# Performance work log

Hardware: AMD Instinct MI355X
Metric: run time of the kernel (lower is better)

## Reference

```python
import jax, jax.numpy as jnp
import numpy as np

TOKENS = 1024
HIDDEN = 1024
INTER = 4096
N_EXPERTS = 8


def setup_inputs() -> dict:
    key = jax.random.key(0)
    k1, k2, k3, k4 = jax.random.split(key, 4)
    hidden_states = jax.random.normal(k1, (TOKENS, HIDDEN), dtype=jnp.float32)
    # multi-hot expert assignment mask [tokens, num_experts] with values in {0,1}
    expert_indices = jax.random.randint(k2, (TOKENS, N_EXPERTS), 0, 2, dtype=jnp.int32)
    # Phi3MLP weights per expert (Linear layers have bias=False in Phi3)
    scale_gu = 1.0 / np.sqrt(HIDDEN)
    scale_d = 1.0 / np.sqrt(INTER)
    w_gate_up = jax.random.normal(k3, (N_EXPERTS, HIDDEN, 2 * INTER), dtype=jnp.float32) * scale_gu
    w_down = jax.random.normal(k4, (N_EXPERTS, INTER, HIDDEN), dtype=jnp.float32) * scale_d
    return {
        "hidden_states": hidden_states,
        "expert_indices": expert_indices,
        "w_gate_up": w_gate_up,
        "w_down": w_down,
    }


def reference(hidden_states, expert_indices, w_gate_up, w_down):
    # Original loops per expert: gather masked tokens, run Phi3MLP, scatter-add back.
    # Mathematically equivalent dense form (jit-friendly, static shapes):
    #   out = sum_e mask[:, e] * Phi3MLP_e(x)
    # gate_up: [E, T, 2*I]
    gu = jnp.einsum('th,ehi->eti', hidden_states, w_gate_up)
    gate, up = jnp.split(gu, 2, axis=-1)  # each [E, T, I]
    act = up * jax.nn.silu(gate)          # Phi3MLP: up * silu(gate)
    y = jnp.einsum('eti,eih->eth', act, w_down)  # [E, T, H]
    mask = expert_indices.astype(hidden_states.dtype)  # [T, E]
    out = jnp.einsum('eth,te->th', y, mask)
    return out
```

## Files before the change

kernel.cpp:

```cpp
#include <hip/hip_runtime.h>
#include <hip/hip_bf16.h>
#include <stdint.h>

#define T_TOK 1024
#define HID   1024
#define INT_  4096
#define NE    8

typedef __attribute__((ext_vector_type(4))) float f32x4;
typedef __attribute__((ext_vector_type(8))) short short8;

__device__ int g_tok[NE][T_TOK];
__device__ int g_cnt[NE];

__device__ __forceinline__ uint32_t pack2bf(float a, float b) {
  unsigned short ua = __builtin_bit_cast(unsigned short, (__bf16)a);
  unsigned short ub = __builtin_bit_cast(unsigned short, (__bf16)b);
  return (uint32_t)ua | ((uint32_t)ub << 16);
}

#define GL16(gsrc, ldst)                                                       \
  __builtin_amdgcn_global_load_lds(                                            \
      (const __attribute__((address_space(1))) void*)(gsrc),                   \
      (__attribute__((address_space(3))) void*)(ldst), 16, 0, 0)

__global__ void k0_compact(const int* __restrict__ mask)
{
  const int w    = threadIdx.x >> 6;
  const int lane = threadIdx.x & 63;
  if (w >= NE) return;
  const unsigned long long ltmask = (1ull << lane) - 1ull;
  int base = 0;
  #pragma unroll
  for (int c = 0; c < T_TOK / 64; ++c) {
    const int t = c * 64 + lane;
    const bool pred = mask[t * NE + w] != 0;
    const unsigned long long bal = __ballot(pred);
    if (pred) g_tok[w][base + __popcll(bal & ltmask)] = t;
    base += __popcll(bal);
  }
  if (lane == 0) g_cnt[w] = base;
}

__global__ void cvt_x(const float* __restrict__ xin, unsigned short* __restrict__ xout)
{
  const int i = (blockIdx.x * 256 + threadIdx.x) * 8;
  f32x4 a = *(const f32x4*)(xin + i);
  f32x4 b = *(const f32x4*)(xin + i + 4);
  uint4 u;
  u.x = pack2bf(a[0], a[1]); u.y = pack2bf(a[2], a[3]);
  u.z = pack2bf(b[0], b[1]); u.w = pack2bf(b[2], b[3]);
  *(uint4*)(xout + i) = u;
}

__global__ void cvt_T(const float* __restrict__ in, unsigned short* __restrict__ out,
                      int R, int C)
{
  __shared__ float tile[64][65];
  const int e  = blockIdx.z;
  const int c0 = blockIdx.x * 64;
  const int r0 = blockIdx.y * 64;
  const float*    ip = in  + (size_t)e * R * C;
  unsigned short* op = out + (size_t)e * R * C;
  const int t  = threadIdx.x;
  const int rr = t >> 4, c4 = (t & 15) * 4;
  #pragma unroll
  for (int s = 0; s < 4; ++s) {
    f32x4 v = *(const f32x4*)(ip + (size_t)(r0 + s * 16 + rr) * C + c0 + c4);
    tile[s * 16 + rr][c4 + 0] = v[0];
    tile[s * 16 + rr][c4 + 1] = v[1];
    tile[s * 16 + rr][c4 + 2] = v[2];
    tile[s * 16 + rr][c4 + 3] = v[3];
  }
  __syncthreads();
  const int c = t >> 2, rs = (t & 3) * 16;
  uint4 u0, u1;
  u0.x = pack2bf(tile[rs + 0][c],  tile[rs + 1][c]);
  u0.y = pack2bf(tile[rs + 2][c],  tile[rs + 3][c]);
  u0.z = pack2bf(tile[rs + 4][c],  tile[rs + 5][c]);
  u0.w = pack2bf(tile[rs + 6][c],  tile[rs + 7][c]);
  u1.x = pack2bf(tile[rs + 8][c],  tile[rs + 9][c]);
  u1.y = pack2bf(tile[rs + 10][c], tile[rs + 11][c]);
  u1.z = pack2bf(tile[rs + 12][c], tile[rs + 13][c]);
  u1.w = pack2bf(tile[rs + 14][c], tile[rs + 15][c]);
  unsigned short* orow = op + (size_t)(c0 + c) * R + r0 + rs;
  *(uint4*)(orow)     = u0;
  *(uint4*)(orow + 8) = u1;
}

__global__ __launch_bounds__(512, 1)
void k1_gateup(const unsigned short* __restrict__ xb,
               const unsigned short* __restrict__ wguT,
               unsigned short* __restrict__ act)
{
  const int e   = blockIdx.z;
  const int cnt = g_cnt[e];
  const int mt  = blockIdx.y;
  const int t0  = mt * 256;
  if (t0 >= cnt) return;

  __shared__ char sA [256 * 128];
  __shared__ char sBg[128 * 128];
  __shared__ char sBu[128 * 128];

  const int nt   = blockIdx.x;
  const int tid  = threadIdx.x;
  const int lane = tid & 63;
  const int wv   = tid >> 6;
  const int wm   = (wv >> 2) * 128;
  const int wn   = (wv & 3) * 32;
  const int n0   = nt * 128;

  const unsigned short* wg = wguT + (size_t)e * 8192 * HID + (size_t)n0 * HID;
  const unsigned short* wu = wg + (size_t)4096 * HID;

  f32x4 accg[8][2], accu[8][2];
  #pragma unroll
  for (int i = 0; i < 8; ++i)
    #pragma unroll
    for (int j = 0; j < 2; ++j) {
      accg[i][j] = (f32x4){0.f, 0.f, 0.f, 0.f};
      accu[i][j] = (f32x4){0.f, 0.f, 0.f, 0.f};
    }

  const int drow  = lane >> 3;
  const int dchk8 = (((lane & 7) ^ drow) << 3);

  int tokA[4];
  #pragma unroll
  for (int s = 0; s < 4; ++s)
    tokA[s] = g_tok[e][t0 + (s * 8 + wv) * 8 + drow];

  for (int kt = 0; kt < HID; kt += 64) {
    #pragma unroll
    for (int s = 0; s < 4; ++s) {
      const int rb = (s * 8 + wv) * 8;
      GL16(xb + (size_t)tokA[s] * HID + kt + dchk8, sA + rb * 128);
    }
    #pragma unroll
    for (int s = 0; s < 2; ++s) {
      const int rb = (s * 8 + wv) * 8;
      GL16(wg + (size_t)(rb + drow) * HID + kt + dchk8, sBg + rb * 128);
      GL16(wu + (size_t)(rb + drow) * HID + kt + dchk8, sBu + rb * 128);
    }
    __syncthreads();
    #pragma unroll
    for (int ks = 0; ks < 2; ++ks) {
      const int kfb = ks * 64 + ((lane >> 4) << 4);
      short8 af[8], bg[2], bu[2];
      #pragma unroll
      for (int i = 0; i < 8; ++i) {
        const int r = wm + i * 16 + (lane & 15);
        af[i] = *(const short8*)(sA + r * 128 + (kfb ^ ((r & 7) << 4)));
      }
      #pragma unroll
      for (int j = 0; j < 2; ++j) {
        const int r = wn + j * 16 + (lane & 15);
        const int off = r * 128 + (kfb ^ ((r & 7) << 4));
        bg[j] = *(const short8*)(sBg + off);
        bu[j] = *(const short8*)(sBu + off);
      }
      #pragma unroll
      for (int i = 0; i < 8; ++i)
        #pragma unroll
        for (int j = 0; j < 2; ++j) {
          accg[i][j] = __builtin_amdgcn_mfma_f32_16x16x32_bf16(af[i], bg[j], accg[i][j], 0, 0, 0);
          accu[i][j] = __builtin_amdgcn_mfma_f32_16x16x32_bf16(af[i], bu[j], accu[i][j], 0, 0, 0);
        }
    }
    __syncthreads();
  }

  unsigned short* ab = act + (size_t)e * T_TOK * INT_;
  #pragma unroll
  for (int i = 0; i < 8; ++i) {
    #pragma unroll
    for (int r = 0; r < 4; ++r) {
      const int slot = t0 + wm + i * 16 + ((lane >> 4) << 2) + r;
      if (slot < cnt) {
        #pragma unroll
        for (int j = 0; j < 2; ++j) {
          const int col = n0 + wn + j * 16 + (lane & 15);
          const float g = accg[i][j][r];
          const float u = accu[i][j][r];
          const float s = u * g / (1.f + __expf(-g));
          ab[(size_t)slot * INT_ + col] = __builtin_bit_cast(unsigned short, (__bf16)s);
        }
      }
    }
  }
}

__global__ __launch_bounds__(256, 2)
void k2_down(const unsigned short* __restrict__ act,
             const unsigned short* __restrict__ wdT,
             float* __restrict__ out)
{
  const int e   = blockIdx.z;
  const int cnt = g_cnt[e];
  const int mt  = blockIdx.y >> 2;
  const int ks4 = blockIdx.y & 3;
  const int t0  = mt * 128;
  if (t0 >= cnt) return;

  __shared__ char sA[128 * 128];
  __shared__ char sB[128 * 128];

  const int nt   = blockIdx.x;
  const int tid  = threadIdx.x;
  const int lane = tid & 63;
  const int wv   = tid >> 6;
  const int wm   = (wv >> 1) * 64;
  const int wn   = (wv & 1) * 64;
  const int n0   = nt * 128;

  const unsigned short* ab = act + (size_t)e * T_TOK * INT_;
  const unsigned short* wb = wdT + (size_t)e * HID * INT_ + (size_t)n0 * INT_;

  f32x4 acc[4][4];
  #pragma unroll
  for (int i = 0; i < 4; ++i)
    #pragma unroll
    for (int j = 0; j < 4; ++j) acc[i][j] = (f32x4){0.f, 0.f, 0.f, 0.f};

  const int drow  = lane >> 3;
  const int dchk8 = (((lane & 7) ^ drow) << 3);

  const int kbeg = ks4 * (INT_ / 4);

  for (int kt = kbeg; kt < kbeg + INT_ / 4; kt += 64) {
    #pragma unroll
    for (int s = 0; s < 4; ++s) {
      const int rb = (s * 4 + wv) * 8;
      GL16(ab + (size_t)(t0 + rb + drow) * INT_ + kt + dchk8, sA + rb * 128);
      GL16(wb + (size_t)(rb + drow) * INT_ + kt + dchk8, sB + rb * 128);
    }
    __syncthreads();
    #pragma unroll
    for (int ks = 0; ks < 2; ++ks) {
      const int kfb = ks * 64 + ((lane >> 4) << 4);
      short8 af[4], bf[4];
      #pragma unroll
      for (int i = 0; i < 4; ++i) {
        const int r = wm + i * 16 + (lane & 15);
        af[i] = *(const short8*)(sA + r * 128 + (kfb ^ ((r & 7) << 4)));
      }
      #pragma unroll
      for (int j = 0; j < 4; ++j) {
        const int r = wn + j * 16 + (lane & 15);
        bf[j] = *(const short8*)(sB + r * 128 + (kfb ^ ((r & 7) << 4)));
      }
      #pragma unroll
      for (int i = 0; i < 4; ++i)
        #pragma unroll
        for (int j = 0; j < 4; ++j)
          acc[i][j] = __builtin_amdgcn_mfma_f32_16x16x32_bf16(af[i], bf[j], acc[i][j], 0, 0, 0);
    }
    __syncthreads();
  }

  #pragma unroll
  for (int i = 0; i < 4; ++i) {
    #pragma unroll
    for (int r = 0; r < 4; ++r) {
      const int slot = t0 + wm + i * 16 + ((lane >> 4) << 2) + r;
      if (slot < cnt) {
        const int token = g_tok[e][slot];
        #pragma unroll
        for (int j = 0; j < 4; ++j) {
          const int col = n0 + wn + j * 16 + (lane & 15);
          atomicAdd(out + (size_t)token * HID + col, acc[i][j][r]);
        }
      }
    }
  }
}

extern "C" void kernel_launch(void* const* d_in, const int* in_sizes, int n_in,
                              void* d_out, int out_size, void* d_ws, size_t ws_size,
                              hipStream_t stream) {
  const float* x   = (const float*)d_in[0];
  const int*   idx = (const int*)d_in[1];
  const float* wgu = (const float*)d_in[2];
  const float* wd  = (const float*)d_in[3];
  float* out = (float*)d_out;

  char* ws = (char*)d_ws;
  unsigned short* act  = (unsigned short*)(ws);
  unsigned short* xb16 = (unsigned short*)(ws + 67108864);
  unsigned short* wguT = (unsigned short*)(ws + 69206016);
  unsigned short* wdT  = (unsigned short*)(ws + 203423744);

  hipMemsetAsync(d_out, 0, (size_t)out_size * sizeof(float), stream);

  k0_compact<<<1, 512, 0, stream>>>(idx);
  cvt_x<<<T_TOK * HID / (256 * 8), 256, 0, stream>>>(x, xb16);
  cvt_T<<<dim3(8192 / 64, 1024 / 64, NE), 256, 0, stream>>>(wgu, wguT, 1024, 8192);
  cvt_T<<<dim3(1024 / 64, 4096 / 64, NE), 256, 0, stream>>>(wd, wdT, 4096, 1024);

  dim3 g1(INT_ / 128, T_TOK / 256, NE);
  k1_gateup<<<g1, dim3(512), 0, stream>>>(xb16, wguT, act);

  dim3 g2(HID / 128, (T_TOK / 128) * 4, NE);
  k2_down<<<g2, dim3(256), 0, stream>>>(act, wdT, out);
}
```

Measured before the change: 366.4 us.

## Double-buffer LDS tiles in gate-up and down GEMM kernels

Both GEMM kernels now keep two LDS buffers per operand and issue the async global-to-LDS loads for the next K tile before computing on the current one. This lets memory latency overlap with MFMA work instead of stalling at each barrier. It doubles shared-memory use: k1 goes to 128KB and k2 to 64KB per block, which may lower occupancy for k2 at two blocks per CU. It also relies on a single barrier per iteration for correctness.

```diff
diff --git a/kernel.cpp b/kernel.cpp
--- a/kernel.cpp
+++ b/kernel.cpp
@@ -99,9 +99,9 @@
   const int t0  = mt * 256;
   if (t0 >= cnt) return;
 
-  __shared__ char sA [256 * 128];
-  __shared__ char sBg[128 * 128];
-  __shared__ char sBu[128 * 128];
+  __shared__ char sA [2][256 * 128];
+  __shared__ char sBg[2][128 * 128];
+  __shared__ char sBu[2][128 * 128];
 
   const int nt   = blockIdx.x;
   const int tid  = threadIdx.x;
@@ -131,19 +131,28 @@
   for (int s = 0; s < 4; ++s)
     tokA[s] = g_tok[e][t0 + (s * 8 + wv) * 8 + drow];
 
-  for (int kt = 0; kt < HID; kt += 64) {
-    #pragma unroll
-    for (int s = 0; s < 4; ++s) {
-      const int rb = (s * 8 + wv) * 8;
-      GL16(xb + (size_t)tokA[s] * HID + kt + dchk8, sA + rb * 128);
-    }
-    #pragma unroll
-    for (int s = 0; s < 2; ++s) {
-      const int rb = (s * 8 + wv) * 8;
-      GL16(wg + (size_t)(rb + drow) * HID + kt + dchk8, sBg + rb * 128);
-      GL16(wu + (size_t)(rb + drow) * HID + kt + dchk8, sBu + rb * 128);
-    }
-    __syncthreads();
+#define K1_STAGE(B, KT)                                                        \
+  do {                                                                         \
+    _Pragma("unroll")                                                          \
+    for (int s_ = 0; s_ < 4; ++s_) {                                           \
+      const int rb_ = (s_ * 8 + wv) * 8;                                       \
+      GL16(xb + (size_t)tokA[s_] * HID + (KT) + dchk8, sA[B] + rb_ * 128);     \
+    }                                                                          \
+    _Pragma("unroll")                                                          \
+    for (int s_ = 0; s_ < 2; ++s_) {                                           \
+      const int rb_ = (s_ * 8 + wv) * 8;                                       \
+      GL16(wg + (size_t)(rb_ + drow) * HID + (KT) + dchk8, sBg[B] + rb_ * 128);\
+      GL16(wu + (size_t)(rb_ + drow) * HID + (KT) + dchk8, sBu[B] + rb_ * 128);\
+    }                                                                          \
+  } while (0)
+
+  K1_STAGE(0, 0);
+  __syncthreads();
+
+  #pragma unroll 2
+  for (int t = 0; t < 16; ++t) {
+    const int cur = t & 1;
+    if (t < 15) K1_STAGE((t + 1) & 1, (t + 1) * 64);
     #pragma unroll
     for (int ks = 0; ks < 2; ++ks) {
       const int kfb = ks * 64 + ((lane >> 4) << 4);
@@ -151,14 +160,14 @@
       #pragma unroll
       for (int i = 0; i < 8; ++i) {
         const int r = wm + i * 16 + (lane & 15);
-        af[i] = *(const short8*)(sA + r * 128 + (kfb ^ ((r & 7) << 4)));
+        af[i] = *(const short8*)(sA[cur] + r * 128 + (kfb ^ ((r & 7) << 4)));
       }
       #pragma unroll
       for (int j = 0; j < 2; ++j) {
         const int r = wn + j * 16 + (lane & 15);
         const int off = r * 128 + (kfb ^ ((r & 7) << 4));
-        bg[j] = *(const short8*)(sBg + off);
-        bu[j] = *(const short8*)(sBu + off);
+        bg[j] = *(const short8*)(sBg[cur] + off);
+        bu[j] = *(const short8*)(sBu[cur] + off);
       }
       #pragma unroll
       for (int i = 0; i < 8; ++i)
@@ -170,6 +179,7 @@
     }
     __syncthreads();
   }
+#undef K1_STAGE
 
   unsigned short* ab = act + (size_t)e * T_TOK * INT_;
   #pragma unroll
@@ -203,8 +213,8 @@
   const int t0  = mt * 128;
   if (t0 >= cnt) return;
 
-  __shared__ char sA[128 * 128];
-  __shared__ char sB[128 * 128];
+  __shared__ char sA[2][128 * 128];
+  __shared__ char sB[2][128 * 128];
 
   const int nt   = blockIdx.x;
   const int tid  = threadIdx.x;
@@ -225,17 +235,25 @@
 
   const int drow  = lane >> 3;
   const int dchk8 = (((lane & 7) ^ drow) << 3);
-
-  const int kbeg = ks4 * (INT_ / 4);
-
-  for (int kt = kbeg; kt < kbeg + INT_ / 4; kt += 64) {
-    #pragma unroll
-    for (int s = 0; s < 4; ++s) {
-      const int rb = (s * 4 + wv) * 8;
-      GL16(ab + (size_t)(t0 + rb + drow) * INT_ + kt + dchk8, sA + rb * 128);
-      GL16(wb + (size_t)(rb + drow) * INT_ + kt + dchk8, sB + rb * 128);
-    }
-    __syncthreads();
+  const int kbeg  = ks4 * (INT_ / 4);
+
+#define K2_STAGE(B, KT)                                                        \
+  do {                                                                         \
+    _Pragma("unroll")                                                          \
+    for (int s_ = 0; s_ < 4; ++s_) {                                           \
+      const int rb_ = (s_ * 4 + wv) * 8;                                       \
+      GL16(ab + (size_t)(t0 + rb_ + drow) * INT_ + (KT) + dchk8, sA[B] + rb_ * 128); \
+      GL16(wb + (size_t)(rb_ + drow) * INT_ + (KT) + dchk8, sB[B] + rb_ * 128);      \
+    }                                                                          \
+  } while (0)
+
+  K2_STAGE(0, kbeg);
+  __syncthreads();
+
+  #pragma unroll 2
+  for (int t = 0; t < 16; ++t) {
+    const int cur = t & 1;
+    if (t < 15) K2_STAGE((t + 1) & 1, kbeg + (t + 1) * 64);
     #pragma unroll
     for (int ks = 0; ks < 2; ++ks) {
       const int kfb = ks * 64 + ((lane >> 4) << 4);
@@ -243,12 +261,12 @@
       #pragma unroll
       for (int i = 0; i < 4; ++i) {
         const int r = wm + i * 16 + (lane & 15);
-        af[i] = *(const short8*)(sA + r * 128 + (kfb ^ ((r & 7) << 4)));
+        af[i] = *(const short8*)(sA[cur] + r * 128 + (kfb ^ ((r & 7) << 4)));
       }
       #pragma unroll
       for (int j = 0; j < 4; ++j) {
         const int r = wn + j * 16 + (lane & 15);
-        bf[j] = *(const short8*)(sB + r * 128 + (kfb ^ ((r & 7) << 4)));
+        bf[j] = *(const short8*)(sB[cur] + r * 128 + (kfb ^ ((r & 7) << 4)));
       }
       #pragma unroll
       for (int i = 0; i < 4; ++i)
@@ -258,6 +276,7 @@
     }
     __syncthreads();
   }
+#undef K2_STAGE
 
   #pragma unroll
   for (int i = 0; i < 4; ++i) {
```

New measurement: 362.7 us. Within noise of the previous version (-1.0%).
